# Optimization experiments

Measured on AMD Instinct MI355X. Metric: run time of the kernel, lower is better.

The kernel has to match this reference:

```python
import jax, jax.numpy as jnp
import numpy as np

MAXK = 5

def _l2norm(x, axis):
    return x / jnp.maximum(jnp.linalg.norm(x, axis=axis, keepdims=True), 1e-12)

def _conv3x3(x, w, b):
    y = jax.lax.conv_general_dilated(x, w, (1, 1), [(1, 1), (1, 1)],
                                     dimension_numbers=('NCHW', 'OIHW', 'NCHW'))
    return y + b[None, :, None, None]

def _bilinear_resize(img, oh, ow):
    # img: [C, ih, iw]; torch F.interpolate(mode='bilinear', align_corners=False)
    ih, iw = img.shape[-2], img.shape[-1]
    def co(o, i):
        src = jnp.clip((jnp.arange(o, dtype=jnp.float32) + 0.5) * (i / o) - 0.5, 0.0, i - 1.0)
        i0 = jnp.floor(src).astype(jnp.int32)
        i1 = jnp.minimum(i0 + 1, i - 1)
        return i0, i1, src - i0
    y0, y1, wy = co(oh, ih)
    x0, x1, wx = co(ow, iw)
    a = img[:, y0][:, :, x0]; b = img[:, y0][:, :, x1]
    c = img[:, y1][:, :, x0]; d = img[:, y1][:, :, x1]
    top = a * (1 - wx) + b * wx
    bot = c * (1 - wx) + d * wx
    return top * (1 - wy[:, None]) + bot * wy[:, None]

def _pos_encode(x, ms, w, b):
    n, _, h, wd = x.shape
    lin = jnp.linspace(-1.0, 1.0, ms)
    gx, gy = jnp.meshgrid(lin, lin, indexing='ij')
    pg = _bilinear_resize(jnp.stack([gx, gy], 0), h, wd)  # [2, h, wd]
    return x + _conv3x3(jnp.broadcast_to(pg[None], (n, 2, h, wd)), w, b)

def _unfold(x, k, s, p):
    # torch F.unfold ordering: channel index = c*k*k + i*k + j
    n, c, h, w = x.shape
    xp = jnp.pad(x, ((0, 0), (0, 0), (p, p), (p, p)))
    oh = (h + 2 * p - k) // s + 1
    ow = (w + 2 * p - k) // s + 1
    cols = [xp[:, :, i:i + oh * s:s, j:j + ow * s:s] for i in range(k) for j in range(k)]
    return jnp.stack(cols, 2).reshape(n, c * k * k, oh * ow)

def _fold(t, c, k, s, p, out_h, out_w):
    n = t.shape[0]
    oh = (out_h + 2 * p - k) // s + 1
    ow = (out_w + 2 * p - k) // s + 1
    pt = t.reshape(n, c, k, k, oh, ow)
    out = jnp.zeros((n, c, out_h + 2 * p, out_w + 2 * p), t.dtype)
    for i in range(k):
        for j in range(k):
            out = out.at[:, :, i:i + oh * s:s, j:j + ow * s:s].add(pt[:, :, i, j])
    return out[:, :, p:p + out_h, p:p + out_w]

def _se(x, w1, b1, w2, b2):
    y = x.mean((2, 3))
    y = jax.nn.sigmoid(jax.nn.relu(y @ w1.T + b1) @ w2.T + b2)
    return x * y[:, :, None, None]

def reference(lrsr_lv3, refsr_lv3, ref_lv1, ref_lv2, ref_lv3,
              k_logits, temperature, global_weight,
              pos_w1, pos_b1, pos_w2, pos_b2, pos_w3, pos_b3,
              se1_w1, se1_b1, se1_w2, se1_b2,
              se2_w1, se2_b1, se2_w2, se2_b2,
              se3_w1, se3_b1, se3_w2, se3_b2):
    N, C, H, W = lrsr_lv3.shape
    HW = H * W
    refsr_enc = _pos_encode(refsr_lv3, 64, pos_w3, pos_b3)
    refsr_n = _l2norm(_unfold(refsr_enc, 3, 1, 1).transpose(0, 2, 1), 2)  # [N, HW, C*9]
    lrsr_n = _l2norm(_unfold(lrsr_lv3, 3, 1, 1), 1)                        # [N, C*9, HW]
    R_local = refsr_n @ lrsr_n                                             # [N, HW, HW]
    ref_g = _l2norm(refsr_enc.mean((2, 3)), 1)
    lr_g = _l2norm(lrsr_lv3.mean((2, 3)), 1)
    R_glob = jnp.sum(ref_g * lr_g, 1)[:, None, None]
    R_comb = (1.0 - global_weight) * R_local + global_weight * R_glob
    # DynamicKSelector: gumbel-softmax with fixed noise key for determinism
    u = jax.random.uniform(jax.random.key(42), k_logits.shape, jnp.float32, 1e-6, 1.0)
    g = -jnp.log(-jnp.log(u))
    k_probs = jax.nn.softmax((k_logits + g) / temperature, -1)
    k_hard = jnp.argmax(k_probs, -1) + 1  # [num_levels]
    # topk(max_k) once; per-level mask with -inf values / 0 indices == original pad
    vals, idx = jax.lax.top_k(R_comb.transpose(0, 2, 1), MAXK)  # [N, HW, K]
    R_star_full = vals.transpose(0, 2, 1)  # [N, K, HW]
    R_idx_full = idx.transpose(0, 2, 1)

    def transfer(ref_feat, lvl, ms, pw, pb, kern, s, p):
        rf = _pos_encode(ref_feat, ms, pw, pb)
        ru = _unfold(rf, kern, s, p)  # [N, C*kern^2, HW]
        mask = (jnp.arange(MAXK) < k_hard[lvl])[None, :, None]
        Rs = jnp.where(mask, R_star_full, -jnp.inf)  # sigmoid(-inf)=0 -> padded rows vanish
        Ri = jnp.where(mask, R_idx_full, 0)
        T_all = jnp.zeros((N, ru.shape[1], HW), ru.dtype)
        for i in range(MAXK):  # small fixed loop over k candidates
            sel = jnp.take_along_axis(ru, Ri[:, i][:, None, :], axis=2)
            T_all = T_all + sel * jax.nn.sigmoid(Rs[:, i])[:, None, :]
        return _fold(T_all, ref_feat.shape[1], kern, s, p, H * s, W * s) / float(kern * kern)

    T3 = transfer(ref_lv3, 0, 64, pos_w3, pos_b3, 3, 1, 1)
    T2 = transfer(ref_lv2, 1, 128, pos_w2, pos_b2, 6, 2, 2)
    T1 = transfer(ref_lv1, 2, 256, pos_w1, pos_b1, 12, 4, 4)
    T3 = _se(T3, se3_w1, se3_b1, se3_w2, se3_b2)
    T2 = _se(T2, se2_w1, se2_b1, se2_w2, se2_b2)
    T1 = _se(T1, se1_w1, se1_b1, se1_w2, se1_b2)
    return (T3, T2, T1)

def setup_inputs():
    key = jax.random.key(0)
    ks = jax.random.split(key, 16)
    N, H, W = 2, 48, 48
    f = jnp.float32
    d = {}
    d['lrsr_lv3'] = jax.random.normal(ks[0], (N, 256, H, W), f)
    d['refsr_lv3'] = jax.random.normal(ks[1], (N, 256, H, W), f)
    d['ref_lv1'] = jax.random.normal(ks[2], (N, 64, 4 * H, 4 * W), f)
    d['ref_lv2'] = jax.random.normal(ks[3], (N, 128, 2 * H, 2 * W), f)
    d['ref_lv3'] = jax.random.normal(ks[4], (N, 256, H, W), f)
    d['k_logits'] = jax.random.normal(ks[5], (3, 5), f)
    d['temperature'] = jnp.array(1.0, f)
    d['global_weight'] = jnp.array(0.1, f)
    for nm, c, i in [('1', 64, 6), ('2', 128, 7), ('3', 256, 8)]:
        d['pos_w' + nm] = jax.random.normal(ks[i], (c, 2, 3, 3), f) * 0.01
        d['pos_b' + nm] = jnp.zeros((c,), f)
    for nm, c, i in [('1', 64, 9), ('2', 128, 10), ('3', 256, 11)]:
        r = c // 16
        k1, k2 = jax.random.split(ks[i])
        d['se' + nm + '_w1'] = jax.random.normal(k1, (r, c), f) / np.sqrt(c).astype(np.float32)
        d['se' + nm + '_b1'] = jnp.zeros((r,), f)
        d['se' + nm + '_w2'] = jax.random.normal(k2, (c, r), f) / np.sqrt(r).astype(np.float32)
        d['se' + nm + '_b2'] = jnp.zeros((c,), f)
    return d
```

## Files before the change

kernel.cpp:

```cpp
#include <hip/hip_runtime.h>
#include <cstdint>
#include <cmath>

#define HW48 2304
#define F9   2304

typedef _Float16 half8_t __attribute__((ext_vector_type(8)));
typedef float floatx4 __attribute__((ext_vector_type(4)));

__device__ __forceinline__ void gl2lds16(const _Float16* g, _Float16* l) {
  __builtin_amdgcn_global_load_lds((const __attribute__((address_space(1))) void*)g,
                                   (__attribute__((address_space(3))) void*)l,
                                   16, 0, 0);
}

__global__ void enc_kernel(const float* __restrict__ src, const float* __restrict__ w,
                           const float* __restrict__ b, float* __restrict__ dst,
                           int C, int H, int ms, int total) {
  int idx = blockIdx.x * blockDim.x + threadIdx.x;
  if (idx >= total) return;
  int x = idx % H;
  int y = (idx / H) % H;
  int c = (idx / (H * H)) % C;
  float scale = (float)((double)ms / (double)H);
  float msm1 = (float)(ms - 1);
  float conv = b[c];
#pragma unroll
  for (int dy = 0; dy < 3; ++dy) {
    int yy = y + dy - 1;
    if (yy < 0 || yy >= H) continue;
    float sy = fminf(fmaxf((yy + 0.5f) * scale - 0.5f, 0.0f), msm1);
    float g0 = -1.0f + 2.0f * sy / msm1;
#pragma unroll
    for (int dx = 0; dx < 3; ++dx) {
      int xx = x + dx - 1;
      if (xx < 0 || xx >= H) continue;
      float sx = fminf(fmaxf((xx + 0.5f) * scale - 0.5f, 0.0f), msm1);
      float g1 = -1.0f + 2.0f * sx / msm1;
      conv += w[((c * 2 + 0) * 3 + dy) * 3 + dx] * g0
            + w[((c * 2 + 1) * 3 + dy) * 3 + dx] * g1;
    }
  }
  dst[idx] = src[idx] + conv;
}

__global__ void unfold_norm_kernel(const float* __restrict__ src,
                                   _Float16* __restrict__ dhi,
                                   _Float16* __restrict__ dlo) {
  int pos = blockIdx.x;
  int n = blockIdx.y;
  int y = pos / 48, x = pos - (pos / 48) * 48;
  int tid = threadIdx.x;
  const float* s = src + (size_t)n * 256 * HW48;
  float v[9];
  float ss = 0.0f;
#pragma unroll
  for (int it = 0; it < 9; ++it) {
    int f = tid + it * 256;
    int c = f / 9, r = f - c * 9;
    int dy = r / 3, dx = r - dy * 3;
    int yy = y + dy - 1, xx = x + dx - 1;
    float val = 0.0f;
    if (yy >= 0 && yy < 48 && xx >= 0 && xx < 48)
      val = s[(c * 48 + yy) * 48 + xx];
    v[it] = val;
    ss += val * val;
  }
  __shared__ float red[256];
  red[tid] = ss;
  __syncthreads();
  for (int ofs = 128; ofs > 0; ofs >>= 1) {
    if (tid < ofs) red[tid] += red[tid + ofs];
    __syncthreads();
  }
  float norm = fmaxf(sqrtf(red[0]), 1e-12f);
  _Float16* dh = dhi + ((size_t)n * HW48 + pos) * (size_t)F9;
  _Float16* dl = dlo + ((size_t)n * HW48 + pos) * (size_t)F9;
#pragma unroll
  for (int it = 0; it < 9; ++it) {
    int f = tid + it * 256;
    float xv = v[it] / norm;
    _Float16 h = (_Float16)xv;
    dh[f] = h;
    dl[f] = (_Float16)(xv - (float)h);
  }
}

__global__ void chmean_kernel(const float* __restrict__ src, float* __restrict__ out, int C, int HW) {
  int c = blockIdx.x, n = blockIdx.y;
  const float* s = src + ((size_t)n * C + c) * HW;
  float sum = 0.0f;
  for (int i = threadIdx.x; i < HW; i += blockDim.x) sum += s[i];
  __shared__ float red[256];
  red[threadIdx.x] = sum;
  __syncthreads();
  for (int ofs = 128; ofs > 0; ofs >>= 1) {
    if (threadIdx.x < ofs) red[threadIdx.x] += red[threadIdx.x + ofs];
    __syncthreads();
  }
  if (threadIdx.x == 0) out[n * C + c] = red[0] / (float)HW;
}

__global__ void rglob_kernel(const float* __restrict__ mref, const float* __restrict__ mlr,
                             float* __restrict__ rg) {
  int n = blockIdx.x;
  int tid = threadIdx.x;
  float a = mref[n * 256 + tid];
  float b = mlr[n * 256 + tid];
  __shared__ float raa[256], rbb[256], rab[256];
  raa[tid] = a * a; rbb[tid] = b * b; rab[tid] = a * b;
  __syncthreads();
  for (int ofs = 128; ofs > 0; ofs >>= 1) {
    if (tid < ofs) { raa[tid] += raa[tid + ofs]; rbb[tid] += rbb[tid + ofs]; rab[tid] += rab[tid + ofs]; }
    __syncthreads();
  }
  if (tid == 0) {
    float na = fmaxf(sqrtf(raa[0]), 1e-12f);
    float nb = fmaxf(sqrtf(rbb[0]), 1e-12f);
    rg[n] = rab[0] / (na * nb);
  }
}

__device__ inline unsigned rotl32(unsigned v, int r) { return (v << r) | (v >> (32 - r)); }

__global__ void khard_kernel(const float* __restrict__ k_logits, const float* __restrict__ temp,
                             int* __restrict__ kh) {
  if (threadIdx.x != 0 || blockIdx.x != 0) return;
  const unsigned ksa[3] = {0u, 42u, 0u ^ 42u ^ 0x1BD11BDAu};
  const int R0[4] = {13, 15, 26, 6};
  const int R1[4] = {17, 29, 16, 24};
  float T = temp[0];
  for (int lvl = 0; lvl < 3; ++lvl) {
    int best = 0;
    float bv = -1e30f;
    for (int j = 0; j < 5; ++j) {
      int idx = lvl * 5 + j;
      unsigned x0 = 0u + ksa[0];
      unsigned x1 = (unsigned)idx + ksa[1];
      for (int grp = 0; grp < 5; ++grp) {
        const int* rr = (grp & 1) ? R1 : R0;
        for (int q = 0; q < 4; ++q) { x0 += x1; x1 = rotl32(x1, rr[q]); x1 ^= x0; }
        x0 += ksa[(grp + 1) % 3];
        x1 += ksa[(grp + 2) % 3] + (unsigned)(grp + 1);
      }
      unsigned bb = x0 ^ x1;
      float f = __uint_as_float((bb >> 9) | 0x3f800000u) - 1.0f;
      float u = __fadd_rn(__fmul_rn(f, 1.0f - 1e-6f), 1e-6f);
      u = fmaxf(u, 1e-6f);
      float g = -logf(-logf(u));
      float v = (k_logits[idx] + g) / T;
      if (v > bv) { bv = v; best = j; }
    }
    kh[lvl] = best + 1;
  }
}

__global__ __launch_bounds__(256) void gemm_mfma_kernel(
    const _Float16* __restrict__ Ah, const _Float16* __restrict__ Al,
    const _Float16* __restrict__ Bh, const _Float16* __restrict__ Bl,
    float* __restrict__ C, const float* __restrict__ rg, const float* __restrict__ gwp) {
  __shared__ __align__(16) _Float16 As_h[128 * 32];
  __shared__ __align__(16) _Float16 As_l[128 * 32];
  __shared__ __align__(16) _Float16 Bs_h[128 * 32];
  __shared__ __align__(16) _Float16 Bs_l[128 * 32];
  const int n = blockIdx.z;
  const size_t nb = (size_t)n * HW48 * F9;
  const _Float16* Ahp = Ah + nb + (size_t)(blockIdx.y * 128) * F9;
  const _Float16* Alp = Al + nb + (size_t)(blockIdx.y * 128) * F9;
  const _Float16* Bhp = Bh + nb + (size_t)(blockIdx.x * 128) * F9;
  const _Float16* Blp = Bl + nb + (size_t)(blockIdx.x * 128) * F9;
  const int tid = threadIdx.x;
  const int lane = tid & 63, wid = tid >> 6;
  const int wm = (wid >> 1) * 64, wn = (wid & 1) * 64;
  const int r16 = lane & 15, quad = lane >> 4;

  int srow[2], sgoff[2], sldsb[2];
#pragma unroll
  for (int s = 0; s < 2; ++s) {
    int row = wid * 32 + s * 16 + (lane >> 2);
    int g = (lane & 3) ^ (row & 3) ^ ((row >> 2) & 3);
    srow[s] = row;
    sgoff[s] = row * F9 + g * 8;
    sldsb[s] = (wid * 32 + s * 16) * 32;
  }

  floatx4 acc[4][4];
#pragma unroll
  for (int i = 0; i < 4; ++i)
#pragma unroll
    for (int j = 0; j < 4; ++j) acc[i][j] = (floatx4){0.f, 0.f, 0.f, 0.f};

  int fa[4], fb[4];
#pragma unroll
  for (int i = 0; i < 4; ++i) {
    int Ra = wm + i * 16 + r16;
    fa[i] = Ra * 32 + ((quad ^ (Ra & 3) ^ ((Ra >> 2) & 3)) * 8);
    int Rb = wn + i * 16 + r16;
    fb[i] = Rb * 32 + ((quad ^ (Rb & 3) ^ ((Rb >> 2) & 3)) * 8);
  }

  for (int k0 = 0; k0 < F9; k0 += 32) {
    __syncthreads();
#pragma unroll
    for (int s = 0; s < 2; ++s) {
      int go = sgoff[s] + k0;
      gl2lds16(Ahp + go, &As_h[sldsb[s]]);
      gl2lds16(Alp + go, &As_l[sldsb[s]]);
      gl2lds16(Bhp + go, &Bs_h[sldsb[s]]);
      gl2lds16(Blp + go, &Bs_l[sldsb[s]]);
    }
    __syncthreads();
    half8_t ah[4], al[4], bh[4], bl[4];
#pragma unroll
    for (int i = 0; i < 4; ++i) {
      ah[i] = *(const half8_t*)&As_h[fa[i]];
      al[i] = *(const half8_t*)&As_l[fa[i]];
      bh[i] = *(const half8_t*)&Bs_h[fb[i]];
      bl[i] = *(const half8_t*)&Bs_l[fb[i]];
    }
#pragma unroll
    for (int i = 0; i < 4; ++i)
#pragma unroll
      for (int j = 0; j < 4; ++j) {
        acc[i][j] = __builtin_amdgcn_mfma_f32_16x16x32_f16(ah[i], bh[j], acc[i][j], 0, 0, 0);
        acc[i][j] = __builtin_amdgcn_mfma_f32_16x16x32_f16(ah[i], bl[j], acc[i][j], 0, 0, 0);
        acc[i][j] = __builtin_amdgcn_mfma_f32_16x16x32_f16(al[i], bh[j], acc[i][j], 0, 0, 0);
      }
  }
  float gw = gwp[0];
  float base = gw * rg[n];
  float w1 = 1.0f - gw;
  float* Cp = C + (size_t)n * HW48 * HW48;
#pragma unroll
  for (int i = 0; i < 4; ++i) {
#pragma unroll
    for (int j = 0; j < 4; ++j) {
#pragma unroll
      for (int r = 0; r < 4; ++r) {
        int row = blockIdx.y * 128 + wm + i * 16 + quad * 4 + r;
        int col = blockIdx.x * 128 + wn + j * 16 + r16;
        Cp[(size_t)row * HW48 + col] = w1 * acc[i][j][r] + base;
      }
    }
  }
}

__global__ __launch_bounds__(256) void topk_kernel(const float* __restrict__ R,
                                                   float2* __restrict__ WP) {
  const int n = blockIdx.y;
  const int tq = threadIdx.x & 15;
  const int tp = threadIdx.x >> 4;
  const int q = blockIdx.x * 16 + tq;
  const float* Rp = R + (size_t)n * HW48 * HW48 + q;
  float v0 = -3.0e38f, v1 = v0, v2 = v0, v3 = v0, v4 = v0;
  int i0 = 0, i1 = 0, i2 = 0, i3 = 0, i4 = 0;
  const int pbeg = tp * 144, pend = pbeg + 144;
  for (int p = pbeg; p < pend; ++p) {
    float val = Rp[(size_t)p * HW48];
    if (val > v4) {
      if (val > v0)      { v4=v3;i4=i3; v3=v2;i3=i2; v2=v1;i2=i1; v1=v0;i1=i0; v0=val;i0=p; }
      else if (val > v1) { v4=v3;i4=i3; v3=v2;i3=i2; v2=v1;i2=i1; v1=val;i1=p; }
      else if (val > v2) { v4=v3;i4=i3; v3=v2;i3=i2; v2=val;i2=p; }
      else if (val > v3) { v4=v3;i4=i3; v3=val;i3=p; }
      else               { v4=val;i4=p; }
    }
  }
  __shared__ float cv[16][16][5];
  __shared__ int   ci[16][16][5];
  cv[tq][tp][0] = v0; ci[tq][tp][0] = i0;
  cv[tq][tp][1] = v1; ci[tq][tp][1] = i1;
  cv[tq][tp][2] = v2; ci[tq][tp][2] = i2;
  cv[tq][tp][3] = v3; ci[tq][tp][3] = i3;
  cv[tq][tp][4] = v4; ci[tq][tp][4] = i4;
  __syncthreads();
  if (tp == 0) {
    float w0 = -3.0e38f, w1 = w0, w2 = w0, w3 = w0, w4 = w0;
    int j0 = 0, j1 = 0, j2 = 0, j3 = 0, j4 = 0;
    for (int s = 0; s < 16; ++s) {
#pragma unroll
      for (int j = 0; j < 5; ++j) {
        float val = cv[tq][s][j];
        int   pi  = ci[tq][s][j];
        if (val > w4) {
          if (val > w0)      { w4=w3;j4=j3; w3=w2;j3=j2; w2=w1;j2=j1; w1=w0;j1=j0; w0=val;j0=pi; }
          else if (val > w1) { w4=w3;j4=j3; w3=w2;j3=j2; w2=w1;j2=j1; w1=val;j1=pi; }
          else if (val > w2) { w4=w3;j4=j3; w3=w2;j3=j2; w2=val;j2=pi; }
          else if (val > w3) { w4=w3;j4=j3; w3=val;j3=pi; }
          else               { w4=val;j4=pi; }
        }
      }
    }
    float2* o = WP + ((size_t)n * HW48 + q) * 5;
    o[0] = make_float2(1.0f / (1.0f + expf(-w0)), __int_as_float(((j0 % 48) << 16) | (j0 / 48)));
    o[1] = make_float2(1.0f / (1.0f + expf(-w1)), __int_as_float(((j1 % 48) << 16) | (j1 / 48)));
    o[2] = make_float2(1.0f / (1.0f + expf(-w2)), __int_as_float(((j2 % 48) << 16) | (j2 / 48)));
    o[3] = make_float2(1.0f / (1.0f + expf(-w3)), __int_as_float(((j3 % 48) << 16) | (j3 / 48)));
    o[4] = make_float2(1.0f / (1.0f + expf(-w4)), __int_as_float(((j4 % 48) << 16) | (j4 / 48)));
  }
}

__global__ __launch_bounds__(256) void transfer_kernel(const float* __restrict__ refenc,
                                                       const float2* __restrict__ WP,
                                                       const int* __restrict__ khp,
                                                       float* __restrict__ out, int C, int s,
                                                       int pad, int lvl, float kk, int total) {
  __shared__ float2 wp_s[1920];
  const int Hout = 48 * s;
  const int HH = Hout * Hout;
  const int idx = blockIdx.x * 256 + threadIdx.x;
  const int sp0 = (blockIdx.x * 256) % HH;
  const int Y0 = sp0 / Hout, Y1 = (sp0 + 255) / Hout;
  const int qh0 = max(0, (Y0 + pad) / s - 2);
  const int qh1 = min(47, (Y1 + pad) / s);
  const int nload = (qh1 - qh0 + 1) * 240;
  const int nblk = (blockIdx.x * 256) / (C * HH);
  const float2* WPn = WP + (size_t)nblk * HW48 * 5 + (size_t)qh0 * 240;
  for (int i = threadIdx.x; i < nload; i += 256) wp_s[i] = WPn[i];
  __syncthreads();
  if (idx >= total) return;

  const int sp = idx % HH;
  const int X = sp % Hout, Y = sp / Hout;
  const int c = (idx / HH) % C;
  const int n = idx / (C * HH);
  const int kh = khp[lvl];
  const int Yp = Y + pad, Xp = X + pad;
  const int Qy = Yp / s, Qx = Xp / s;
  const float* rf = refenc + ((size_t)n * C + c) * (size_t)HH;
  float acc = 0.0f;
  for (int t = 0; t < 3; ++t) {
    int qh = Qy - t;
    if (qh < 0 || qh >= 48) continue;
    int i = Yp - s * qh;
    for (int u = 0; u < 3; ++u) {
      int qw = Qx - u;
      if (qw < 0 || qw >= 48) continue;
      int j = Xp - s * qw;
      int base = ((qh - qh0) * 48 + qw) * 5;
      for (int m = 0; m < kh; ++m) {
        float2 wp = wp_s[base + m];
        float wgt = wp.x;
        int pxy = __float_as_int(wp.y);
        int ph = pxy & 0xffff, pw = pxy >> 16;
        int yy = ph * s + i - pad;
        int xx = pw * s + j - pad;
        if (yy >= 0 && yy < Hout && xx >= 0 && xx < Hout)
          acc = fmaf(wgt, rf[yy * Hout + xx], acc);
      }
    }
  }
  out[idx] = acc / kk;
}

__global__ void se_mlp_kernel(const float* __restrict__ means, const float* __restrict__ w1,
                              const float* __restrict__ b1, const float* __restrict__ w2,
                              const float* __restrict__ b2, float* __restrict__ scale,
                              int C, int R) {
  int n = blockIdx.x;
  int tid = threadIdx.x;
  __shared__ float ym[256];
  __shared__ float h1[16];
  if (tid < C) ym[tid] = means[n * C + tid];
  __syncthreads();
  if (tid < R) {
    float s = b1[tid];
    for (int c = 0; c < C; ++c) s += ym[c] * w1[tid * C + c];
    h1[tid] = fmaxf(s, 0.0f);
  }
  __syncthreads();
  if (tid < C) {
    float s = b2[tid];
    for (int r = 0; r < R; ++r) s += h1[r] * w2[tid * R + r];
    scale[n * C + tid] = 1.0f / (1.0f + expf(-s));
  }
}

__global__ void se_scale_kernel(float* __restrict__ T, const float* __restrict__ scale,
                                int C, int HW, int total) {
  int idx = blockIdx.x * blockDim.x + threadIdx.x;
  if (idx >= total) return;
  int c = (idx / HW) % C;
  int n = idx / (C * HW);
  T[idx] *= scale[n * C + c];
}

extern "C" void kernel_launch(void* const* d_in, const int* in_sizes, int n_in,
                              void* d_out, int out_size, void* d_ws, size_t ws_size,
                              hipStream_t stream) {
  const float* lrsr   = (const float*)d_in[0];
  const float* refsr  = (const float*)d_in[1];
  const float* ref1   = (const float*)d_in[2];
  const float* ref2   = (const float*)d_in[3];
  const float* ref3   = (const float*)d_in[4];
  const float* klog   = (const float*)d_in[5];
  const float* temp   = (const float*)d_in[6];
  const float* gwp    = (const float*)d_in[7];
  const float* pos_w1 = (const float*)d_in[8];
  const float* pos_b1 = (const float*)d_in[9];
  const float* pos_w2 = (const float*)d_in[10];
  const float* pos_b2 = (const float*)d_in[11];
  const float* pos_w3 = (const float*)d_in[12];
  const float* pos_b3 = (const float*)d_in[13];
  const float* se1_w1 = (const float*)d_in[14];
  const float* se1_b1 = (const float*)d_in[15];
  const float* se1_w2 = (const float*)d_in[16];
  const float* se1_b2 = (const float*)d_in[17];
  const float* se2_w1 = (const float*)d_in[18];
  const float* se2_b1 = (const float*)d_in[19];
  const float* se2_w2 = (const float*)d_in[20];
  const float* se2_b2 = (const float*)d_in[21];
  const float* se3_w1 = (const float*)d_in[22];
  const float* se3_b1 = (const float*)d_in[23];
  const float* se3_w2 = (const float*)d_in[24];
  const float* se3_b2 = (const float*)d_in[25];
  float* out = (float*)d_out;
  float* ws = (float*)d_ws;

  float* refsr_enc = ws + 0;
  float* ref3_enc  = ws + 1179648;
  float* ref2_enc  = ws + 2359296;
  float* ref1_enc  = ws + 4718592;
  _Float16* Ah_hi  = (_Float16*)(ws + 9437184);
  _Float16* Ah_lo  = (_Float16*)(ws + 14745600);
  _Float16* Bh_hi  = (_Float16*)(ws + 20054016);
  _Float16* Bh_lo  = (_Float16*)(ws + 25362432);
  float* Rm        = ws + 30670848;
  float2* WP       = (float2*)(ws + 41287680);
  float* mref      = ws + 41333760;
  float* mlr       = ws + 41334272;
  float* rg        = ws + 41334784;
  int*   kh        = (int*)(ws + 41334788);
  float* semean    = ws + 41334792;
  float* sescale   = ws + 41335304;

  float* T3 = out;
  float* T2 = out + 1179648;
  float* T1 = out + 3538944;

  enc_kernel<<<4608, 256, 0, stream>>>(refsr, pos_w3, pos_b3, refsr_enc, 256, 48, 64, 1179648);
  enc_kernel<<<4608, 256, 0, stream>>>(ref3, pos_w3, pos_b3, ref3_enc, 256, 48, 64, 1179648);
  enc_kernel<<<9216, 256, 0, stream>>>(ref2, pos_w2, pos_b2, ref2_enc, 128, 96, 128, 2359296);
  enc_kernel<<<18432, 256, 0, stream>>>(ref1, pos_w1, pos_b1, ref1_enc, 64, 192, 256, 4718592);

  unfold_norm_kernel<<<dim3(2304, 2), 256, 0, stream>>>(refsr_enc, Ah_hi, Ah_lo);
  unfold_norm_kernel<<<dim3(2304, 2), 256, 0, stream>>>(lrsr, Bh_hi, Bh_lo);

  chmean_kernel<<<dim3(256, 2), 256, 0, stream>>>(refsr_enc, mref, 256, 2304);
  chmean_kernel<<<dim3(256, 2), 256, 0, stream>>>(lrsr, mlr, 256, 2304);
  rglob_kernel<<<2, 256, 0, stream>>>(mref, mlr, rg);
  khard_kernel<<<1, 64, 0, stream>>>(klog, temp, kh);

  gemm_mfma_kernel<<<dim3(18, 18, 2), 256, 0, stream>>>(Ah_hi, Ah_lo, Bh_hi, Bh_lo, Rm, rg, gwp);

  topk_kernel<<<dim3(144, 2), 256, 0, stream>>>(Rm, WP);

  transfer_kernel<<<4608, 256, 0, stream>>>(ref3_enc, WP, kh, T3, 256, 1, 1, 0, 9.0f, 1179648);
  transfer_kernel<<<9216, 256, 0, stream>>>(ref2_enc, WP, kh, T2, 128, 2, 2, 1, 36.0f, 2359296);
  transfer_kernel<<<18432, 256, 0, stream>>>(ref1_enc, WP, kh, T1, 64, 4, 4, 2, 144.0f, 4718592);

  chmean_kernel<<<dim3(256, 2), 256, 0, stream>>>(T3, semean, 256, 2304);
  se_mlp_kernel<<<2, 256, 0, stream>>>(semean, se3_w1, se3_b1, se3_w2, se3_b2, sescale, 256, 16);
  se_scale_kernel<<<4608, 256, 0, stream>>>(T3, sescale, 256, 2304, 1179648);

  chmean_kernel<<<dim3(128, 2), 256, 0, stream>>>(T2, semean, 128, 9216);
  se_mlp_kernel<<<2, 256, 0, stream>>>(semean, se2_w1, se2_b1, se2_w2, se2_b2, sescale, 128, 8);
  se_scale_kernel<<<9216, 256, 0, stream>>>(T2, sescale, 128, 9216, 2359296);

  chmean_kernel<<<dim3(64, 2), 256, 0, stream>>>(T1, semean, 64, 36864);
  se_mlp_kernel<<<2, 256, 0, stream>>>(semean, se1_w1, se1_b1, se1_w2, se1_b2, sescale, 64, 4);
  se_scale_kernel<<<18432, 256, 0, stream>>>(T1, sescale, 64, 36864, 4718592);
}
```

Before: 1.017 ms.

## Use channel-last layout for reference features in texture transfer and SE

The positional-encoding kernels for the reference levels now write channels-last tensors. The transfer kernel maps 64 consecutive channels to a wavefront so each gathered patch read is coalesced across channels, and it reads weights/positions directly from global memory instead of staging them in LDS. Transfer outputs go to a channels-last scratch buffer. SE means are computed with a strided atomic reduction, and a tiled transpose-and-scale kernel writes the final NCHW output. This replaces uncoalesced spatial gathers with an extra transpose pass, added atomics, and memsets.

```diff
diff --git a/kernel.cpp b/kernel.cpp
--- a/kernel.cpp
+++ b/kernel.cpp
@@ -44,6 +44,37 @@
   dst[idx] = src[idx] + conv;
 }
 
+__global__ void enc_t_kernel(const float* __restrict__ src, const float* __restrict__ w,
+                             const float* __restrict__ b, float* __restrict__ dst,
+                             int C, int H, int ms, int total) {
+  int idx = blockIdx.x * blockDim.x + threadIdx.x;
+  if (idx >= total) return;
+  int c = idx % C;
+  int x = (idx / C) % H;
+  int y = (idx / (C * H)) % H;
+  int n = idx / (C * H * H);
+  float scale = (float)((double)ms / (double)H);
+  float msm1 = (float)(ms - 1);
+  float conv = b[c];
+#pragma unroll
+  for (int dy = 0; dy < 3; ++dy) {
+    int yy = y + dy - 1;
+    if (yy < 0 || yy >= H) continue;
+    float sy = fminf(fmaxf((yy + 0.5f) * scale - 0.5f, 0.0f), msm1);
+    float g0 = -1.0f + 2.0f * sy / msm1;
+#pragma unroll
+    for (int dx = 0; dx < 3; ++dx) {
+      int xx = x + dx - 1;
+      if (xx < 0 || xx >= H) continue;
+      float sx = fminf(fmaxf((xx + 0.5f) * scale - 0.5f, 0.0f), msm1);
+      float g1 = -1.0f + 2.0f * sx / msm1;
+      conv += w[((c * 2 + 0) * 3 + dy) * 3 + dx] * g0
+            + w[((c * 2 + 1) * 3 + dy) * 3 + dx] * g1;
+    }
+  }
+  dst[idx] = src[((size_t)(n * C + c) * H + y) * H + x] + conv;
+}
+
 __global__ void unfold_norm_kernel(const float* __restrict__ src,
                                    _Float16* __restrict__ dhi,
                                    _Float16* __restrict__ dlo) {
@@ -99,6 +130,27 @@
     __syncthreads();
   }
   if (threadIdx.x == 0) out[n * C + c] = red[0] / (float)HW;
+}
+
+__global__ void chmean_t_kernel(const float* __restrict__ T_t, float* __restrict__ sums,
+                                int C, int HH) {
+  int n = blockIdx.y;
+  int S = 256 / C;
+  int c = threadIdx.x % C;
+  int st = threadIdx.x / C;
+  const float* base = T_t + (size_t)n * HH * C;
+  int per = HH / gridDim.x;
+  int sp0 = blockIdx.x * per;
+  float sum = 0.0f;
+  for (int sp = sp0 + st; sp < sp0 + per; sp += S)
+    sum += base[(size_t)sp * C + c];
+  __shared__ float red[256];
+  red[threadIdx.x] = sum;
+  __syncthreads();
+  if (st == 0) {
+    for (int k = 1; k < S; ++k) sum += red[c + k * C];
+    atomicAdd(&sums[n * C + c], sum);
+  }
 }
 
 __global__ void rglob_kernel(const float* __restrict__ mref, const float* __restrict__ mlr,
@@ -174,12 +226,11 @@
   const int wm = (wid >> 1) * 64, wn = (wid & 1) * 64;
   const int r16 = lane & 15, quad = lane >> 4;
 
-  int srow[2], sgoff[2], sldsb[2];
+  int sgoff[2], sldsb[2];
 #pragma unroll
   for (int s = 0; s < 2; ++s) {
     int row = wid * 32 + s * 16 + (lane >> 2);
     int g = (lane & 3) ^ (row & 3) ^ ((row >> 2) & 3);
-    srow[s] = row;
     sgoff[s] = row * F9 + g * 8;
     sldsb[s] = (wid * 32 + s * 16) * 32;
   }
@@ -299,68 +350,58 @@
   }
 }
 
-__global__ __launch_bounds__(256) void transfer_kernel(const float* __restrict__ refenc,
-                                                       const float2* __restrict__ WP,
-                                                       const int* __restrict__ khp,
-                                                       float* __restrict__ out, int C, int s,
-                                                       int pad, int lvl, float kk, int total) {
-  __shared__ float2 wp_s[1920];
-  const int Hout = 48 * s;
+template<int S>
+__global__ __launch_bounds__(256) void transfer_t_kernel(const float* __restrict__ rf_t,
+                                                         const float2* __restrict__ WP,
+                                                         const int* __restrict__ khp,
+                                                         float* __restrict__ out_t,
+                                                         int C, int lvl, float kk) {
+  const int Hout = 48 * S;
   const int HH = Hout * Hout;
-  const int idx = blockIdx.x * 256 + threadIdx.x;
-  const int sp0 = (blockIdx.x * 256) % HH;
-  const int Y0 = sp0 / Hout, Y1 = (sp0 + 255) / Hout;
-  const int qh0 = max(0, (Y0 + pad) / s - 2);
-  const int qh1 = min(47, (Y1 + pad) / s);
-  const int nload = (qh1 - qh0 + 1) * 240;
-  const int nblk = (blockIdx.x * 256) / (C * HH);
-  const float2* WPn = WP + (size_t)nblk * HW48 * 5 + (size_t)qh0 * 240;
-  for (int i = threadIdx.x; i < nload; i += 256) wp_s[i] = WPn[i];
-  __syncthreads();
-  if (idx >= total) return;
-
-  const int sp = idx % HH;
+  const int pad = S;
+  const int g = threadIdx.x >> 6, lane = threadIdx.x & 63;
+  const int sp = blockIdx.x * 4 + g;
+  const int c = blockIdx.y * 64 + lane;
+  const int n = blockIdx.z;
   const int X = sp % Hout, Y = sp / Hout;
-  const int c = (idx / HH) % C;
-  const int n = idx / (C * HH);
   const int kh = khp[lvl];
   const int Yp = Y + pad, Xp = X + pad;
-  const int Qy = Yp / s, Qx = Xp / s;
-  const float* rf = refenc + ((size_t)n * C + c) * (size_t)HH;
+  const int Qy = Yp / S, Qx = Xp / S;
+  const float* rf = rf_t + (size_t)n * HH * C;
+  const float2* Wq = WP + (size_t)n * HW48 * 5;
   float acc = 0.0f;
   for (int t = 0; t < 3; ++t) {
     int qh = Qy - t;
     if (qh < 0 || qh >= 48) continue;
-    int i = Yp - s * qh;
+    int i = Yp - S * qh;
     for (int u = 0; u < 3; ++u) {
       int qw = Qx - u;
       if (qw < 0 || qw >= 48) continue;
-      int j = Xp - s * qw;
-      int base = ((qh - qh0) * 48 + qw) * 5;
+      int j = Xp - S * qw;
+      int qb = (qh * 48 + qw) * 5;
       for (int m = 0; m < kh; ++m) {
-        float2 wp = wp_s[base + m];
-        float wgt = wp.x;
+        float2 wp = Wq[qb + m];
         int pxy = __float_as_int(wp.y);
         int ph = pxy & 0xffff, pw = pxy >> 16;
-        int yy = ph * s + i - pad;
-        int xx = pw * s + j - pad;
+        int yy = ph * S + i - pad;
+        int xx = pw * S + j - pad;
         if (yy >= 0 && yy < Hout && xx >= 0 && xx < Hout)
-          acc = fmaf(wgt, rf[yy * Hout + xx], acc);
+          acc = fmaf(wp.x, rf[(size_t)(yy * Hout + xx) * C + c], acc);
       }
     }
   }
-  out[idx] = acc / kk;
-}
-
-__global__ void se_mlp_kernel(const float* __restrict__ means, const float* __restrict__ w1,
+  out_t[(size_t)n * HH * C + (size_t)sp * C + c] = acc / kk;
+}
+
+__global__ void se_mlp_kernel(const float* __restrict__ sums, const float* __restrict__ w1,
                               const float* __restrict__ b1, const float* __restrict__ w2,
                               const float* __restrict__ b2, float* __restrict__ scale,
-                              int C, int R) {
+                              int C, int R, float invHH) {
   int n = blockIdx.x;
   int tid = threadIdx.x;
   __shared__ float ym[256];
   __shared__ float h1[16];
-  if (tid < C) ym[tid] = means[n * C + tid];
+  if (tid < C) ym[tid] = sums[n * C + tid] * invHH;
   __syncthreads();
   if (tid < R) {
     float s = b1[tid];
@@ -375,13 +416,27 @@
   }
 }
 
-__global__ void se_scale_kernel(float* __restrict__ T, const float* __restrict__ scale,
-                                int C, int HW, int total) {
-  int idx = blockIdx.x * blockDim.x + threadIdx.x;
-  if (idx >= total) return;
-  int c = (idx / HW) % C;
-  int n = idx / (C * HW);
-  T[idx] *= scale[n * C + c];
+__global__ __launch_bounds__(256) void transpose_scale_kernel(const float* __restrict__ T_t,
+                                                              const float* __restrict__ scale,
+                                                              float* __restrict__ out,
+                                                              int C, int HH) {
+  __shared__ float tile[64][65];
+  int n = blockIdx.z;
+  int sp0 = blockIdx.x * 64, c0 = blockIdx.y * 64;
+  int tc = threadIdx.x & 63, ts = threadIdx.x >> 6;
+  const float* src = T_t + (size_t)n * HH * C;
+#pragma unroll
+  for (int i = 0; i < 16; ++i) {
+    int spl = ts * 16 + i;
+    tile[tc][spl] = src[(size_t)(sp0 + spl) * C + c0 + tc];
+  }
+  __syncthreads();
+#pragma unroll
+  for (int i = 0; i < 16; ++i) {
+    int cl = ts * 16 + i;
+    float s = scale[n * C + c0 + cl];
+    out[((size_t)n * C + c0 + cl) * HH + sp0 + tc] = tile[cl][tc] * s;
+  }
 }
 
 extern "C" void kernel_launch(void* const* d_in, const int* in_sizes, int n_in,
@@ -416,21 +471,24 @@
   float* out = (float*)d_out;
   float* ws = (float*)d_ws;
 
-  float* refsr_enc = ws + 0;
-  float* ref3_enc  = ws + 1179648;
-  float* ref2_enc  = ws + 2359296;
-  float* ref1_enc  = ws + 4718592;
+  float* refsr_enc  = ws + 0;
+  float* ref3_enc_t = ws + 1179648;
+  float* ref2_enc_t = ws + 2359296;
+  float* ref1_enc_t = ws + 4718592;
   _Float16* Ah_hi  = (_Float16*)(ws + 9437184);
   _Float16* Ah_lo  = (_Float16*)(ws + 14745600);
   _Float16* Bh_hi  = (_Float16*)(ws + 20054016);
   _Float16* Bh_lo  = (_Float16*)(ws + 25362432);
   float* Rm        = ws + 30670848;
+  float* T3t = ws + 30670848;
+  float* T2t = ws + 31850496;
+  float* T1t = ws + 34209792;
   float2* WP       = (float2*)(ws + 41287680);
   float* mref      = ws + 41333760;
   float* mlr       = ws + 41334272;
   float* rg        = ws + 41334784;
   int*   kh        = (int*)(ws + 41334788);
-  float* semean    = ws + 41334792;
+  float* sesum     = ws + 41334792;
   float* sescale   = ws + 41335304;
 
   float* T3 = out;
@@ -438,9 +496,9 @@
   float* T1 = out + 3538944;
 
   enc_kernel<<<4608, 256, 0, stream>>>(refsr, pos_w3, pos_b3, refsr_enc, 256, 48, 64, 1179648);
-  enc_kernel<<<4608, 256, 0, stream>>>(ref3, pos_w3, pos_b3, ref3_enc, 256, 48, 64, 1179648);
-  enc_kernel<<<9216, 256, 0, stream>>>(ref2, pos_w2, pos_b2, ref2_enc, 128, 96, 128, 2359296);
-  enc_kernel<<<18432, 256, 0, stream>>>(ref1, pos_w1, pos_b1, ref1_enc, 64, 192, 256, 4718592);
+  enc_t_kernel<<<4608, 256, 0, stream>>>(ref3, pos_w3, pos_b3, ref3_enc_t, 256, 48, 64, 1179648);
+  enc_t_kernel<<<9216, 256, 0, stream>>>(ref2, pos_w2, pos_b2, ref2_enc_t, 128, 96, 128, 2359296);
+  enc_t_kernel<<<18432, 256, 0, stream>>>(ref1, pos_w1, pos_b1, ref1_enc_t, 64, 192, 256, 4718592);
 
   unfold_norm_kernel<<<dim3(2304, 2), 256, 0, stream>>>(refsr_enc, Ah_hi, Ah_lo);
   unfold_norm_kernel<<<dim3(2304, 2), 256, 0, stream>>>(lrsr, Bh_hi, Bh_lo);
@@ -454,19 +512,22 @@
 
   topk_kernel<<<dim3(144, 2), 256, 0, stream>>>(Rm, WP);
 
-  transfer_kernel<<<4608, 256, 0, stream>>>(ref3_enc, WP, kh, T3, 256, 1, 1, 0, 9.0f, 1179648);
-  transfer_kernel<<<9216, 256, 0, stream>>>(ref2_enc, WP, kh, T2, 128, 2, 2, 1, 36.0f, 2359296);
-  transfer_kernel<<<18432, 256, 0, stream>>>(ref1_enc, WP, kh, T1, 64, 4, 4, 2, 144.0f, 4718592);
-
-  chmean_kernel<<<dim3(256, 2), 256, 0, stream>>>(T3, semean, 256, 2304);
-  se_mlp_kernel<<<2, 256, 0, stream>>>(semean, se3_w1, se3_b1, se3_w2, se3_b2, sescale, 256, 16);
-  se_scale_kernel<<<4608, 256, 0, stream>>>(T3, sescale, 256, 2304, 1179648);
-
-  chmean_kernel<<<dim3(128, 2), 256, 0, stream>>>(T2, semean, 128, 9216);
-  se_mlp_kernel<<<2, 256, 0, stream>>>(semean, se2_w1, se2_b1, se2_w2, se2_b2, sescale, 128, 8);
-  se_scale_kernel<<<9216, 256, 0, stream>>>(T2, sescale, 128, 9216, 2359296);
-
-  chmean_kernel<<<dim3(64, 2), 256, 0, stream>>>(T1, semean, 64, 36864);
-  se_mlp_kernel<<<2, 256, 0, stream>>>(semean, se1_w1, se1_b1, se1_w2, se1_b2, sescale, 64, 4);
-  se_scale_kernel<<<18432, 256, 0, stream>>>(T1, sescale, 64, 36864, 4718592);
-}
+  transfer_t_kernel<1><<<dim3(576, 4, 2), 256, 0, stream>>>(ref3_enc_t, WP, kh, T3t, 256, 0, 9.0f);
+  transfer_t_kernel<2><<<dim3(2304, 2, 2), 256, 0, stream>>>(ref2_enc_t, WP, kh, T2t, 128, 1, 36.0f);
+  transfer_t_kernel<4><<<dim3(9216, 1, 2), 256, 0, stream>>>(ref1_enc_t, WP, kh, T1t, 64, 2, 144.0f);
+
+  hipMemsetAsync(sesum, 0, 512 * sizeof(float), stream);
+  chmean_t_kernel<<<dim3(16, 2), 256, 0, stream>>>(T3t, sesum, 256, 2304);
+  se_mlp_kernel<<<2, 256, 0, stream>>>(sesum, se3_w1, se3_b1, se3_w2, se3_b2, sescale, 256, 16, 1.0f / 2304.0f);
+  transpose_scale_kernel<<<dim3(36, 4, 2), 256, 0, stream>>>(T3t, sescale, T3, 256, 2304);
+
+  hipMemsetAsync(sesum, 0, 512 * sizeof(float), stream);
+  chmean_t_kernel<<<dim3(16, 2), 256, 0, stream>>>(T2t, sesum, 128, 9216);
+  se_mlp_kernel<<<2, 256, 0, stream>>>(sesum, se2_w1, se2_b1, se2_w2, se2_b2, sescale, 128, 8, 1.0f / 9216.0f);
+  transpose_scale_kernel<<<dim3(144, 2, 2), 256, 0, stream>>>(T2t, sescale, T2, 128, 9216);
+
+  hipMemsetAsync(sesum, 0, 512 * sizeof(float), stream);
+  chmean_t_kernel<<<dim3(16, 2), 256, 0, stream>>>(T1t, sesum, 64, 36864);
+  se_mlp_kernel<<<2, 256, 0, stream>>>(sesum, se1_w1, se1_b1, se1_w2, se1_b2, sescale, 64, 4, 1.0f / 36864.0f);
+  transpose_scale_kernel<<<dim3(576, 1, 2), 256, 0, stream>>>(T1t, sescale, T1, 64, 36864);
+}
```

Result: slower. 1.201 ms (+18.1%).

## Fuse per-tile top-5 selection into GEMM epilogue and add small merge kernel

Applied to the files above, without the earlier changes.

The GEMM no longer writes the full 2304x2304 correlation matrix per batch. Each block instead computes a per-column top-5 over its 128 rows, using registers and then LDS, and writes only those candidates. A small merge kernel then combines the 18 row-tiles per column, applies the global-weight affine transform, and runs the sigmoid. This removes roughly 42 MB of correlation writes and rereads plus the strided top-k scan, at the cost of extra epilogue work and syncs inside the GEMM. Ties are now broken toward the lower row index, and the affine transform is applied after selection, which keeps the ordering only while 1-gw is positive.

```diff
diff --git a/kernel.cpp b/kernel.cpp
--- a/kernel.cpp
+++ b/kernel.cpp
@@ -12,6 +12,16 @@
   __builtin_amdgcn_global_load_lds((const __attribute__((address_space(1))) void*)g,
                                    (__attribute__((address_space(3))) void*)l,
                                    16, 0, 0);
+}
+
+__device__ __forceinline__ void insert5(float v, int row, float* tv, int* tr) {
+  if (v > tv[4] || (v == tv[4] && row < tr[4])) {
+    int k = 4;
+    while (k > 0 && (v > tv[k - 1] || (v == tv[k - 1] && row < tr[k - 1]))) {
+      tv[k] = tv[k - 1]; tr[k] = tr[k - 1]; --k;
+    }
+    tv[k] = v; tr[k] = row;
+  }
 }
 
 __global__ void enc_kernel(const float* __restrict__ src, const float* __restrict__ w,
@@ -158,7 +168,7 @@
 __global__ __launch_bounds__(256) void gemm_mfma_kernel(
     const _Float16* __restrict__ Ah, const _Float16* __restrict__ Al,
     const _Float16* __restrict__ Bh, const _Float16* __restrict__ Bl,
-    float* __restrict__ C, const float* __restrict__ rg, const float* __restrict__ gwp) {
+    float2* __restrict__ tileTop) {
   __shared__ __align__(16) _Float16 As_h[128 * 32];
   __shared__ __align__(16) _Float16 As_l[128 * 32];
   __shared__ __align__(16) _Float16 Bs_h[128 * 32];
@@ -174,12 +184,11 @@
   const int wm = (wid >> 1) * 64, wn = (wid & 1) * 64;
   const int r16 = lane & 15, quad = lane >> 4;
 
-  int srow[2], sgoff[2], sldsb[2];
+  int sgoff[2], sldsb[2];
 #pragma unroll
   for (int s = 0; s < 2; ++s) {
     int row = wid * 32 + s * 16 + (lane >> 2);
     int g = (lane & 3) ^ (row & 3) ^ ((row >> 2) & 3);
-    srow[s] = row;
     sgoff[s] = row * F9 + g * 8;
     sldsb[s] = (wid * 32 + s * 16) * 32;
   }
@@ -227,75 +236,74 @@
         acc[i][j] = __builtin_amdgcn_mfma_f32_16x16x32_f16(al[i], bh[j], acc[i][j], 0, 0, 0);
       }
   }
-  float gw = gwp[0];
-  float base = gw * rg[n];
-  float w1 = 1.0f - gw;
-  float* Cp = C + (size_t)n * HW48 * HW48;
-#pragma unroll
-  for (int i = 0; i < 4; ++i) {
-#pragma unroll
-    for (int j = 0; j < 4; ++j) {
-#pragma unroll
-      for (int r = 0; r < 4; ++r) {
-        int row = blockIdx.y * 128 + wm + i * 16 + quad * 4 + r;
-        int col = blockIdx.x * 128 + wn + j * 16 + r16;
-        Cp[(size_t)row * HW48 + col] = w1 * acc[i][j][r] + base;
-      }
-    }
-  }
-}
-
-__global__ __launch_bounds__(256) void topk_kernel(const float* __restrict__ R,
-                                                   float2* __restrict__ WP) {
-  const int n = blockIdx.y;
-  const int tq = threadIdx.x & 15;
-  const int tp = threadIdx.x >> 4;
-  const int q = blockIdx.x * 16 + tq;
-  const float* Rp = R + (size_t)n * HW48 * HW48 + q;
-  float v0 = -3.0e38f, v1 = v0, v2 = v0, v3 = v0, v4 = v0;
-  int i0 = 0, i1 = 0, i2 = 0, i3 = 0, i4 = 0;
-  const int pbeg = tp * 144, pend = pbeg + 144;
-  for (int p = pbeg; p < pend; ++p) {
-    float val = Rp[(size_t)p * HW48];
-    if (val > v4) {
-      if (val > v0)      { v4=v3;i4=i3; v3=v2;i3=i2; v2=v1;i2=i1; v1=v0;i1=i0; v0=val;i0=p; }
-      else if (val > v1) { v4=v3;i4=i3; v3=v2;i3=i2; v2=v1;i2=i1; v1=val;i1=p; }
-      else if (val > v2) { v4=v3;i4=i3; v3=v2;i3=i2; v2=val;i2=p; }
-      else if (val > v3) { v4=v3;i4=i3; v3=val;i3=p; }
-      else               { v4=val;i4=p; }
-    }
-  }
-  __shared__ float cv[16][16][5];
-  __shared__ int   ci[16][16][5];
-  cv[tq][tp][0] = v0; ci[tq][tp][0] = i0;
-  cv[tq][tp][1] = v1; ci[tq][tp][1] = i1;
-  cv[tq][tp][2] = v2; ci[tq][tp][2] = i2;
-  cv[tq][tp][3] = v3; ci[tq][tp][3] = i3;
-  cv[tq][tp][4] = v4; ci[tq][tp][4] = i4;
-  __syncthreads();
-  if (tp == 0) {
-    float w0 = -3.0e38f, w1 = w0, w2 = w0, w3 = w0, w4 = w0;
-    int j0 = 0, j1 = 0, j2 = 0, j3 = 0, j4 = 0;
-    for (int s = 0; s < 16; ++s) {
-#pragma unroll
-      for (int j = 0; j < 5; ++j) {
-        float val = cv[tq][s][j];
-        int   pi  = ci[tq][s][j];
-        if (val > w4) {
-          if (val > w0)      { w4=w3;j4=j3; w3=w2;j3=j2; w2=w1;j2=j1; w1=w0;j1=j0; w0=val;j0=pi; }
-          else if (val > w1) { w4=w3;j4=j3; w3=w2;j3=j2; w2=w1;j2=j1; w1=val;j1=pi; }
-          else if (val > w2) { w4=w3;j4=j3; w3=w2;j3=j2; w2=val;j2=pi; }
-          else if (val > w3) { w4=w3;j4=j3; w3=val;j3=pi; }
-          else               { w4=val;j4=pi; }
+
+  float* evals = (float*)As_h;
+  int*   erows = (int*)As_l;
+  float2* tout = tileTop + ((((size_t)n * 18 + blockIdx.y) * 18 + blockIdx.x) * 128) * 5;
+  const int rowbase = blockIdx.y * 128 + wm;
+  for (int j = 0; j < 4; ++j) {
+    float tv[5]; int tr[5];
+#pragma unroll
+    for (int k = 0; k < 5; ++k) { tv[k] = -3.0e38f; tr[k] = 0x7fffffff; }
+#pragma unroll
+    for (int i = 0; i < 4; ++i)
+#pragma unroll
+      for (int r = 0; r < 4; ++r)
+        insert5(acc[i][j][r], rowbase + i * 16 + quad * 4 + r, tv, tr);
+    __syncthreads();
+#pragma unroll
+    for (int k = 0; k < 5; ++k) {
+      evals[tid * 5 + k] = tv[k];
+      erows[tid * 5 + k] = tr[k];
+    }
+    __syncthreads();
+    if (tid < 32) {
+      int wnq = tid >> 4;
+      int rr = tid & 15;
+      float mv[5]; int mr[5];
+#pragma unroll
+      for (int k = 0; k < 5; ++k) { mv[k] = -3.0e38f; mr[k] = 0x7fffffff; }
+      for (int wsel = 0; wsel < 2; ++wsel) {
+        int lbase = (wnq + wsel * 2) * 64 + rr;
+        for (int qd = 0; qd < 4; ++qd) {
+          int lidx = lbase + qd * 16;
+#pragma unroll
+          for (int k = 0; k < 5; ++k)
+            insert5(evals[lidx * 5 + k], erows[lidx * 5 + k], mv, mr);
         }
       }
-    }
-    float2* o = WP + ((size_t)n * HW48 + q) * 5;
-    o[0] = make_float2(1.0f / (1.0f + expf(-w0)), __int_as_float(((j0 % 48) << 16) | (j0 / 48)));
-    o[1] = make_float2(1.0f / (1.0f + expf(-w1)), __int_as_float(((j1 % 48) << 16) | (j1 / 48)));
-    o[2] = make_float2(1.0f / (1.0f + expf(-w2)), __int_as_float(((j2 % 48) << 16) | (j2 / 48)));
-    o[3] = make_float2(1.0f / (1.0f + expf(-w3)), __int_as_float(((j3 % 48) << 16) | (j3 / 48)));
-    o[4] = make_float2(1.0f / (1.0f + expf(-w4)), __int_as_float(((j4 % 48) << 16) | (j4 / 48)));
+      float2* o = tout + (size_t)(wnq * 64 + j * 16 + rr) * 5;
+#pragma unroll
+      for (int k = 0; k < 5; ++k) o[k] = make_float2(mv[k], __int_as_float(mr[k]));
+    }
+  }
+}
+
+__global__ void topk_merge_kernel(const float2* __restrict__ tileTop,
+                                  const float* __restrict__ rg, const float* __restrict__ gwp,
+                                  float2* __restrict__ WP) {
+  int t = blockIdx.x * 256 + threadIdx.x;
+  if (t >= 2 * HW48) return;
+  int n = t / HW48, q = t % HW48;
+  int bx = q >> 7, c = q & 127;
+  float mv[5]; int mr[5];
+#pragma unroll
+  for (int k = 0; k < 5; ++k) { mv[k] = -3.0e38f; mr[k] = 0x7fffffff; }
+  for (int by = 0; by < 18; ++by) {
+    const float2* src = tileTop + ((((size_t)n * 18 + by) * 18 + bx) * 128 + c) * 5;
+#pragma unroll
+    for (int k = 0; k < 5; ++k) {
+      float2 e = src[k];
+      insert5(e.x, __float_as_int(e.y), mv, mr);
+    }
+  }
+  float gw = gwp[0], base = gw * rg[n], w1 = 1.0f - gw;
+  float2* o = WP + ((size_t)n * HW48 + q) * 5;
+#pragma unroll
+  for (int k = 0; k < 5; ++k) {
+    float val = w1 * mv[k] + base;
+    int p = mr[k];
+    o[k] = make_float2(1.0f / (1.0f + expf(-val)), __int_as_float(((p % 48) << 16) | (p / 48)));
   }
 }
 
@@ -424,7 +432,7 @@
   _Float16* Ah_lo  = (_Float16*)(ws + 14745600);
   _Float16* Bh_hi  = (_Float16*)(ws + 20054016);
   _Float16* Bh_lo  = (_Float16*)(ws + 25362432);
-  float* Rm        = ws + 30670848;
+  float2* tileTop  = (float2*)(ws + 30670848);
   float2* WP       = (float2*)(ws + 41287680);
   float* mref      = ws + 41333760;
   float* mlr       = ws + 41334272;
@@ -450,9 +458,9 @@
   rglob_kernel<<<2, 256, 0, stream>>>(mref, mlr, rg);
   khard_kernel<<<1, 64, 0, stream>>>(klog, temp, kh);
 
-  gemm_mfma_kernel<<<dim3(18, 18, 2), 256, 0, stream>>>(Ah_hi, Ah_lo, Bh_hi, Bh_lo, Rm, rg, gwp);
-
-  topk_kernel<<<dim3(144, 2), 256, 0, stream>>>(Rm, WP);
+  gemm_mfma_kernel<<<dim3(18, 18, 2), 256, 0, stream>>>(Ah_hi, Ah_lo, Bh_hi, Bh_lo, tileTop);
+
+  topk_merge_kernel<<<18, 256, 0, stream>>>(tileTop, rg, gwp, WP);
 
   transfer_kernel<<<4608, 256, 0, stream>>>(ref3_enc, WP, kh, T3, 256, 1, 1, 0, 9.0f, 1179648);
   transfer_kernel<<<9216, 256, 0, stream>>>(ref2_enc, WP, kh, T2, 128, 2, 2, 1, 36.0f, 2359296);
```

After: 1.555 ms. 1.53x slower.
